# Kernel tuning notes

Hardware: AMD Instinct MI355X
Metric: run time of the kernel (lower is better)

The kernel has to match this reference:

```python
import jax, jax.numpy as jnp
import numpy as np

N_QUBITS = 10


def setup_inputs() -> dict:
    key = jax.random.key(0)
    kx, kw = jax.random.split(key)
    # x: batch of rotation angles, last dim = n_qubits
    x = jax.random.normal(kx, (16384, 256, N_QUBITS), dtype=jnp.float32)
    # trainable per-qubit RY angles (nn.Parameter in the torch module)
    weights = jax.random.normal(kw, (N_QUBITS,), dtype=jnp.float32)
    return {"x": x, "weights": weights}


def reference(x, weights):
    """Exact analytic evaluation of the quantum circuit.

    Circuit: RX(x_i) on wire i, RY(w_i) on wire i, CNOT chain (0,1),(1,2),...,
    then expval(PauliZ(i)) on each wire.

    Derivation: pulling Z_i back through the CNOT chain (CNOT(c,t)^† Z_t
    CNOT(c,t) = Z_c Z_t) gives <Z_i> = <Z_0 Z_1 ... Z_i>. The pre-CNOT state
    is a product state, and for a single qubit RY(w)RX(x)|0> has
    <Z> = cos(x) cos(w). Hence out[..., i] = prod_{j<=i} cos(x_j) cos(w_j),
    i.e. a cumulative product along the qubit axis. This is bit-exact with
    the full state-vector simulation (up to float rounding).
    """
    per_qubit = jnp.cos(x) * jnp.cos(weights)  # [..., n_qubits], weights broadcast
    return jnp.cumprod(per_qubit, axis=-1)      # [..., n_qubits]
```

## Files before the change

### kernel.cpp

```cpp
#include <hip/hip_runtime.h>


#define BLOCK 256
#define WAVES 4
#define NQ 10
#define WQ 320
#define ROWS_PER_WAVE 128

typedef float f32x4 __attribute__((ext_vector_type(4)));

__global__ __launch_bounds__(BLOCK) void qcircuit_kernel(
    const float* __restrict__ x,
    const float* __restrict__ w,
    float* __restrict__ out,
    long long n_rows,
    long long nfull)
{
    __shared__ f32x4 buf[WAVES * WQ];

    const int tid  = threadIdx.x;
    const int wid  = tid >> 6;
    const int lane = tid & 63;
    f32x4* wbuf = buf + wid * WQ;

    const f32x4* __restrict__ gin  = (const f32x4*)x;
    f32x4* __restrict__       gout = (f32x4*)out;

    float cw[NQ];
    #pragma unroll
    for (int j = 0; j < NQ; ++j) cw[j] = __cosf(w[j]);

    const long long wtile = (long long)blockIdx.x * WAVES + wid;

    if (wtile < nfull) {
        const long long base_u4 = wtile * WQ;

        #pragma unroll
        for (int p = 0; p < 5; ++p) {
            __builtin_amdgcn_global_load_lds(
                (const __attribute__((address_space(1))) void*)
                    (gin + base_u4 + p * 64 + lane),
                (__attribute__((address_space(3))) void*)(wbuf + p * 64 + lane),
                16, 0, 0);
        }
        asm volatile("s_waitcnt vmcnt(0)" ::: "memory");
        __builtin_amdgcn_sched_barrier(0);

        float v[20];
        f32x4* vr = (f32x4*)v;
        #pragma unroll
        for (int k = 0; k < 5; ++k) vr[k] = wbuf[lane * 5 + k];

        float pr = 1.0f;
        #pragma unroll
        for (int j = 0; j < NQ; ++j) { pr *= __cosf(v[j]) * cw[j]; v[j] = pr; }
        pr = 1.0f;
        #pragma unroll
        for (int j = 0; j < NQ; ++j) { pr *= __cosf(v[NQ + j]) * cw[j]; v[NQ + j] = pr; }

        #pragma unroll
        for (int k = 0; k < 5; ++k) wbuf[lane * 5 + k] = vr[k];

        asm volatile("s_waitcnt lgkmcnt(0)" ::: "memory");
        __builtin_amdgcn_sched_barrier(0);

        #pragma unroll
        for (int p = 0; p < 5; ++p) {
            f32x4 sv = wbuf[p * 64 + lane];
            gout[base_u4 + p * 64 + lane] = sv;
        }
    }

    if (blockIdx.x == 0 && wid == 0) {
        for (long long r = nfull * ROWS_PER_WAVE + lane; r < n_rows; r += 64) {
            const float* gi = x   + r * NQ;
            float*       go = out + r * NQ;
            float pr = 1.0f;
            #pragma unroll
            for (int j = 0; j < NQ; ++j) { pr *= __cosf(gi[j]) * cw[j]; go[j] = pr; }
        }
    }
}

extern "C" void kernel_launch(void* const* d_in, const int* in_sizes, int n_in,
                              void* d_out, int out_size, void* d_ws, size_t ws_size,
                              hipStream_t stream) {
    const float* x = (const float*)d_in[0];
    const float* w = (const float*)d_in[1];
    float* out = (float*)d_out;

    const long long n_elem = in_sizes[0];
    const long long n_rows = n_elem / NQ;
    const long long total_u4 = (n_rows * NQ) / 4;
    const long long nfull = total_u4 / WQ;
    long long blocks = (nfull + WAVES - 1) / WAVES;
    if (blocks < 1) blocks = 1;

    hipLaunchKernelGGL(qcircuit_kernel, dim3((int)blocks), dim3(BLOCK), 0, stream,
                       x, w, out, n_rows, nfull);
}
```

Before: 282.2 us.

## Make kernel persistent grid-stride with prefetch of next tile into LDS

Caps the grid at a fixed block count and has each wave loop over tiles grid-stride. While it writes back the current tile from registers, it issues async global-to-LDS loads for the next tile, so load latency can overlap with stores and compute. Launch bounds now ask for 8 blocks per CU. This trades the many short-lived blocks for fewer persistent waves, which risks lower memory-level parallelism and adds vmcnt ordering subtleties.

```diff
diff --git a/kernel.cpp b/kernel.cpp
--- a/kernel.cpp
+++ b/kernel.cpp
@@ -5,11 +5,12 @@
 #define WAVES 4
 #define NQ 10
 #define WQ 320
-#define ROWS_PER_WAVE 128
+#define ROWS_PER_TILE 128
+#define MAX_BLOCKS 2048
 
 typedef float f32x4 __attribute__((ext_vector_type(4)));
 
-__global__ __launch_bounds__(BLOCK) void qcircuit_kernel(
+__global__ __launch_bounds__(BLOCK, 8) void qcircuit_kernel(
     const float* __restrict__ x,
     const float* __restrict__ w,
     float* __restrict__ out,
@@ -30,21 +31,27 @@
     #pragma unroll
     for (int j = 0; j < NQ; ++j) cw[j] = __cosf(w[j]);
 
-    const long long wtile = (long long)blockIdx.x * WAVES + wid;
+#define STAGE(t)                                                               \
+    _Pragma("unroll")                                                          \
+    for (int p = 0; p < 5; ++p) {                                              \
+        __builtin_amdgcn_global_load_lds(                                      \
+            (const __attribute__((address_space(1))) void*)                    \
+                (gin + (t) * WQ + p * 64 + lane),                              \
+            (__attribute__((address_space(3))) void*)(wbuf + p * 64 + lane),   \
+            16, 0, 0);                                                         \
+    }
 
-    if (wtile < nfull) {
-        const long long base_u4 = wtile * WQ;
+    const long long nslots = (long long)gridDim.x * WAVES;
+    const long long w0 = (long long)blockIdx.x * WAVES + wid;
 
-        #pragma unroll
-        for (int p = 0; p < 5; ++p) {
-            __builtin_amdgcn_global_load_lds(
-                (const __attribute__((address_space(1))) void*)
-                    (gin + base_u4 + p * 64 + lane),
-                (__attribute__((address_space(3))) void*)(wbuf + p * 64 + lane),
-                16, 0, 0);
-        }
+    if (w0 < nfull) {
+        STAGE(w0);
         asm volatile("s_waitcnt vmcnt(0)" ::: "memory");
-        __builtin_amdgcn_sched_barrier(0);
+    }
+
+    for (long long wt = w0; wt < nfull; wt += nslots) {
+        const long long base = wt * WQ;
+        const long long nx   = wt + nslots;
 
         float v[20];
         f32x4* vr = (f32x4*)v;
@@ -60,19 +67,24 @@
 
         #pragma unroll
         for (int k = 0; k < 5; ++k) wbuf[lane * 5 + k] = vr[k];
+        asm volatile("s_waitcnt lgkmcnt(0)" ::: "memory");
 
+        f32x4 sv[5];
+        #pragma unroll
+        for (int p = 0; p < 5; ++p) sv[p] = wbuf[p * 64 + lane];
         asm volatile("s_waitcnt lgkmcnt(0)" ::: "memory");
+
+        if (nx < nfull) { STAGE(nx); }
         __builtin_amdgcn_sched_barrier(0);
 
         #pragma unroll
-        for (int p = 0; p < 5; ++p) {
-            f32x4 sv = wbuf[p * 64 + lane];
-            gout[base_u4 + p * 64 + lane] = sv;
-        }
+        for (int p = 0; p < 5; ++p) gout[base + p * 64 + lane] = sv[p];
+
+        if (nx < nfull) { asm volatile("s_waitcnt vmcnt(5)" ::: "memory"); }
     }
 
     if (blockIdx.x == 0 && wid == 0) {
-        for (long long r = nfull * ROWS_PER_WAVE + lane; r < n_rows; r += 64) {
+        for (long long r = nfull * ROWS_PER_TILE + lane; r < n_rows; r += 64) {
             const float* gi = x   + r * NQ;
             float*       go = out + r * NQ;
             float pr = 1.0f;
@@ -80,6 +92,7 @@
             for (int j = 0; j < NQ; ++j) { pr *= __cosf(gi[j]) * cw[j]; go[j] = pr; }
         }
     }
+#undef STAGE
 }
 
 extern "C" void kernel_launch(void* const* d_in, const int* in_sizes, int n_in,
@@ -94,6 +107,7 @@
     const long long total_u4 = (n_rows * NQ) / 4;
     const long long nfull = total_u4 / WQ;
     long long blocks = (nfull + WAVES - 1) / WAVES;
+    if (blocks > MAX_BLOCKS) blocks = MAX_BLOCKS;
     if (blocks < 1) blocks = 1;
 
     hipLaunchKernelGGL(qcircuit_kernel, dim3((int)blocks), dim3(BLOCK), 0, stream,
```

Result: no change. 287.2 us (+1.8%).
